# Optimization experiments

Hardware: AMD Instinct MI355X
Metric: run time of the kernel (lower is better)

The kernel has to match this reference:

```python
import jax, jax.numpy as jnp
import numpy as np

LORA_ALPHA = 32
LORA_RANK = 16
SCALING = LORA_ALPHA / LORA_RANK  # 2.0


def setup_inputs() -> dict:
    key = jax.random.key(0)
    ks = jax.random.split(key, 6)
    B_, S, D_IN, D_OUT, E, R = 4, 2048, 4096, 4096, 8, LORA_RANK
    x = jax.random.normal(ks[0], (B_, S, D_IN), dtype=jnp.float32)
    W_base = jax.random.normal(ks[1], (D_OUT, D_IN), dtype=jnp.float32) * (D_IN ** -0.5)
    b_base = jax.random.normal(ks[2], (D_OUT,), dtype=jnp.float32) * 0.01
    W_gate = jax.random.normal(ks[3], (E, D_IN), dtype=jnp.float32) * (D_IN ** -0.5)
    A = jax.random.normal(ks[4], (E, R, D_IN), dtype=jnp.float32) * (D_IN ** -0.5)
    B = jax.random.normal(ks[5], (D_OUT, R), dtype=jnp.float32)[None] * jnp.ones((E, 1, 1), jnp.float32) * 0.02
    B = jax.random.normal(ks[5], (E, D_OUT, R), dtype=jnp.float32) * 0.02
    return {"x": x, "W_base": W_base, "b_base": b_base, "W_gate": W_gate, "A": A, "B": B}


def reference(x, W_base, b_base, W_gate, A, B):
    # Base linear: [b,s,d_in] @ [d_out,d_in]^T -> [b,s,d_out]
    result = jnp.einsum('bsd,od->bso', x, W_base) + b_base
    # Softmax gating over experts: [b,s,E]
    route = jax.nn.softmax(jnp.einsum('bsd,ed->bse', x, W_gate), axis=-1)
    # All-expert low-rank down-projection: [b,s,E,r] (dropout is Identity, p=0)
    h = jnp.einsum('bsd,erd->bser', x, A)
    # Fuse route weight into the small low-rank intermediate before up-projection
    hw = h * route[..., None]
    # Weighted sum over experts of up-projection: [b,s,d_out]
    result = result + SCALING * jnp.einsum('bser,eor->bso', hw, B)
    return result
```

## Files before the change

### kernel.cpp

```cpp
#include <hip/hip_runtime.h>
#include <hip/hip_bf16.h>


typedef __attribute__((ext_vector_type(8))) short  bf16x8;
typedef __attribute__((ext_vector_type(4))) float  f32x4;
typedef __attribute__((ext_vector_type(4))) unsigned short us4;
typedef __attribute__((ext_vector_type(4))) float  fl4;

__device__ __forceinline__ unsigned short f2bf(float f) {
  unsigned int u = __float_as_uint(f);
  u += 0x7FFFu + ((u >> 16) & 1u);
  return (unsigned short)(u >> 16);
}

__device__ __forceinline__ void gload16(const void* g, void* l) {
  __builtin_amdgcn_global_load_lds(
      (const __attribute__((address_space(1))) unsigned int*)g,
      (__attribute__((address_space(3))) unsigned int*)l, 16, 0, 0);
}

#define WS_XBF 0u
#define WS_WBF 67108864u
#define WS_AG  100663296u
#define WS_U   101842944u
#define WS_HW  102891520u

__global__ __launch_bounds__(256) void prep_kernel(
    const float* __restrict__ x, const float* __restrict__ Wb,
    const float* __restrict__ Wg, const float* __restrict__ A,
    const float* __restrict__ B,
    unsigned short* __restrict__ Xbf, unsigned short* __restrict__ Wbf,
    unsigned short* __restrict__ AG, unsigned short* __restrict__ U)
{
  const long N0 = 8388608;
  const long N1 = N0 + 4194304;
  const long N2 = N1 + 139264;
  const long N3 = N2 + 8192;
  const long N4 = N3 + 131072;
  long i = (long)blockIdx.x * blockDim.x + threadIdx.x;
  long stride = (long)gridDim.x * blockDim.x;
  for (; i < N4; i += stride) {
    if (i < N1) {
      const float* s; unsigned short* d; long j;
      if (i < N0) { s = x;  d = Xbf; j = i; }
      else        { s = Wb; d = Wbf; j = i - N0; }
      fl4 v = ((const fl4*)s)[j];
      us4 o; o[0]=f2bf(v[0]); o[1]=f2bf(v[1]); o[2]=f2bf(v[2]); o[3]=f2bf(v[3]);
      ((us4*)d)[j] = o;
    } else if (i < N2) {
      long j = i - N1;
      fl4 v = (j < 8192) ? ((const fl4*)Wg)[j] : ((const fl4*)A)[j - 8192];
      us4 o; o[0]=f2bf(v[0]); o[1]=f2bf(v[1]); o[2]=f2bf(v[2]); o[3]=f2bf(v[3]);
      ((us4*)AG)[j] = o;
    } else if (i < N3) {
      long j = i - N2;
      us4 z = (us4)0;
      ((us4*)(AG + 136*4096))[j] = z;
    } else {
      long j = i - N3;
      long o = j >> 5;
      long c4 = j & 31;
      long e = c4 >> 2, r4 = c4 & 3;
      fl4 v = ((const fl4*)B)[e*16384 + o*4 + r4];
      us4 t; t[0]=f2bf(2.f*v[0]); t[1]=f2bf(2.f*v[1]);
             t[2]=f2bf(2.f*v[2]); t[3]=f2bf(2.f*v[3]);
      ((us4*)U)[j] = t;
    }
  }
}

__global__ __launch_bounds__(256) void gate_h_kernel(
    const unsigned short* __restrict__ Xbf,
    const unsigned short* __restrict__ AG,
    unsigned short* __restrict__ HW)
{
  __shared__ unsigned short Xt[64*32];
  __shared__ unsigned short At[144*32];
  __shared__ float accs[64*136];

  int tid = threadIdx.x;
  int lane = tid & 63;
  int w = tid >> 6;
  long brow = (long)blockIdx.x * 64;

  f32x4 acc[9];
#pragma unroll
  for (int i = 0; i < 9; ++i) acc[i] = (f32x4){0.f,0.f,0.f,0.f};

  int lrow = lane >> 2;
  int lcol = (lane & 3) * 8;

  for (int kb = 0; kb < 128; ++kb) {
    __syncthreads();
    gload16(Xbf + (brow + w*16 + lrow)*4096 + kb*32 + lcol, (char*)Xt + w*1024);
    for (int c = w; c < 9; c += 4)
      gload16(AG + (long)(c*16 + lrow)*4096 + kb*32 + lcol, (char*)At + c*1024);
    __syncthreads();
    int r16 = lane & 15, kh = lane >> 4;
    bf16x8 a = *(const bf16x8*)&Xt[(w*16 + r16)*32 + kh*8];
#pragma unroll
    for (int n = 0; n < 9; ++n) {
      bf16x8 b = *(const bf16x8*)&At[(n*16 + r16)*32 + kh*8];
      acc[n] = __builtin_amdgcn_mfma_f32_16x16x32_bf16(a, b, acc[n], 0, 0, 0);
    }
  }
  __syncthreads();
  {
    int r16 = lane & 15, rg = lane >> 4;
#pragma unroll
    for (int n = 0; n < 9; ++n) {
      int col = n*16 + r16;
      if (col < 136) {
#pragma unroll
        for (int j = 0; j < 4; ++j)
          accs[(w*16 + rg*4 + j)*136 + col] = acc[n][j];
      }
    }
  }
  __syncthreads();
  {
    int r = tid >> 2;
    int q = tid & 3;
    const float* rp = &accs[r*136];
    float mx = rp[0];
#pragma unroll
    for (int e = 1; e < 8; ++e) mx = fmaxf(mx, rp[e]);
    float ex[8]; float s = 0.f;
#pragma unroll
    for (int e = 0; e < 8; ++e) { ex[e] = __expf(rp[e] - mx); s += ex[e]; }
    float inv = 1.f / s;
#pragma unroll
    for (int jj = 0; jj < 8; ++jj) {
      int col = q*32 + jj*4;
      float rt = ex[col >> 4] * inv;
      us4 o;
      o[0] = f2bf(rp[8+col+0] * rt);
      o[1] = f2bf(rp[8+col+1] * rt);
      o[2] = f2bf(rp[8+col+2] * rt);
      o[3] = f2bf(rp[8+col+3] * rt);
      *(us4*)&HW[(brow + r)*128 + col] = o;
    }
  }
}

__global__ __launch_bounds__(256) void gemm_main(
    const unsigned short* __restrict__ Xbf,
    const unsigned short* __restrict__ Wbf,
    const unsigned short* __restrict__ HW,
    const unsigned short* __restrict__ U,
    const float* __restrict__ bias,
    float* __restrict__ out)
{
  __shared__ unsigned short At[128*32];
  __shared__ unsigned short Bt[128*32];

  int tid = threadIdx.x;
  int lane = tid & 63;
  int w = tid >> 6;
  int wr = w >> 1, wc = w & 1;

  int bid = blockIdx.x;
  long brow = (long)(bid >> 5) * 128;
  long bcol = (long)(bid & 31) * 128;

  f32x4 acc[4][4];
#pragma unroll
  for (int m = 0; m < 4; ++m)
#pragma unroll
    for (int n = 0; n < 4; ++n) acc[m][n] = (f32x4){0.f,0.f,0.f,0.f};

  int lrow = lane >> 2;
  int lcol = (lane & 3) * 8;
  int r16 = lane & 15, kh = lane >> 4;

  auto step = [&](const unsigned short* __restrict__ pA, long ldA,
                  const unsigned short* __restrict__ pB, long ldB, int k0) {
    __syncthreads();
#pragma unroll
    for (int i = 0; i < 2; ++i) {
      int chunk = w*2 + i;
      int row = chunk*16 + lrow;
      gload16(pA + (brow + row)*ldA + k0 + lcol, (char*)At + chunk*1024);
      gload16(pB + (bcol + row)*ldB + k0 + lcol, (char*)Bt + chunk*1024);
    }
    __syncthreads();
    bf16x8 af[4], bfr[4];
#pragma unroll
    for (int m = 0; m < 4; ++m)
      af[m] = *(const bf16x8*)&At[(wr*64 + m*16 + r16)*32 + kh*8];
#pragma unroll
    for (int n = 0; n < 4; ++n)
      bfr[n] = *(const bf16x8*)&Bt[(wc*64 + n*16 + r16)*32 + kh*8];
#pragma unroll
    for (int m = 0; m < 4; ++m)
#pragma unroll
      for (int n = 0; n < 4; ++n)
        acc[m][n] = __builtin_amdgcn_mfma_f32_16x16x32_bf16(af[m], bfr[n], acc[m][n], 0, 0, 0);
  };

  for (int kb = 0; kb < 128; ++kb) step(Xbf, 4096, Wbf, 4096, kb*32);
  for (int kb = 0; kb < 4;   ++kb) step(HW, 128, U, 128, kb*32);

  int rg = lane >> 4;
#pragma unroll
  for (int n = 0; n < 4; ++n) {
    long col = bcol + wc*64 + n*16 + r16;
    float b = bias[col];
#pragma unroll
    for (int m = 0; m < 4; ++m) {
      long row0 = brow + wr*64 + m*16 + rg*4;
#pragma unroll
      for (int j = 0; j < 4; ++j)
        out[(row0 + j)*4096 + col] = acc[m][n][j] + b;
    }
  }
}

extern "C" void kernel_launch(void* const* d_in, const int* in_sizes, int n_in,
                              void* d_out, int out_size, void* d_ws, size_t ws_size,
                              hipStream_t stream) {
  (void)in_sizes; (void)n_in; (void)out_size; (void)ws_size;
  const float* x  = (const float*)d_in[0];
  const float* Wb = (const float*)d_in[1];
  const float* bb = (const float*)d_in[2];
  const float* Wg = (const float*)d_in[3];
  const float* A  = (const float*)d_in[4];
  const float* B  = (const float*)d_in[5];
  float* out = (float*)d_out;
  char* ws = (char*)d_ws;

  unsigned short* Xbf = (unsigned short*)(ws + WS_XBF);
  unsigned short* Wbf = (unsigned short*)(ws + WS_WBF);
  unsigned short* AG  = (unsigned short*)(ws + WS_AG);
  unsigned short* U   = (unsigned short*)(ws + WS_U);
  unsigned short* HW  = (unsigned short*)(ws + WS_HW);

  hipLaunchKernelGGL(prep_kernel, dim3(2048), dim3(256), 0, stream,
                     x, Wb, Wg, A, B, Xbf, Wbf, AG, U);
  hipLaunchKernelGGL(gate_h_kernel, dim3(128), dim3(256), 0, stream,
                     Xbf, AG, HW);
  hipLaunchKernelGGL(gemm_main, dim3(2048), dim3(256), 0, stream,
                     Xbf, Wbf, HW, U, bb, out);
}
```

Before: 684.7 us.

## Rewrite main GEMM as 256x256 pipelined tile and split-K the gate kernel

The main GEMM moves from 128x128 tiles with 32-wide K steps to 256x256 tiles with 64-wide K steps, 8 waves per block, double-buffered LDS with an XOR swizzle, and interleaved prefetch/MFMA phases using explicit vmcnt waits and s_setprio. The gate/down-projection kernel is split along K into two halves across 512 blocks, writing bf16 partials that a separate reduce kernel sums before applying the softmax and route scaling. The aim is more data reuse per tile and latency hiding in the dominant GEMM, plus more parallelism in the small gate GEMM. The cost is an extra launch and round trip through memory, and bf16 rounding of the partial logits, which slightly lowers gating precision.

After: 564.2 us. -17.6%, faster.

```diff
diff --git a/kernel.cpp b/kernel.cpp
--- a/kernel.cpp
+++ b/kernel.cpp
@@ -12,18 +12,27 @@
   u += 0x7FFFu + ((u >> 16) & 1u);
   return (unsigned short)(u >> 16);
 }
-
+__device__ __forceinline__ float bf2f(unsigned short u) {
+  return __uint_as_float(((unsigned int)u) << 16);
+}
 __device__ __forceinline__ void gload16(const void* g, void* l) {
   __builtin_amdgcn_global_load_lds(
       (const __attribute__((address_space(1))) unsigned int*)g,
       (__attribute__((address_space(3))) unsigned int*)l, 16, 0, 0);
 }
+
+#define BAR() do { asm volatile("" ::: "memory"); \
+                   __builtin_amdgcn_s_barrier();  \
+                   asm volatile("" ::: "memory"); } while (0)
+#define VMCNT6() asm volatile("s_waitcnt vmcnt(6)" ::: "memory")
+#define VMCNT0() asm volatile("s_waitcnt vmcnt(0)" ::: "memory")
 
 #define WS_XBF 0u
 #define WS_WBF 67108864u
 #define WS_AG  100663296u
 #define WS_U   101842944u
 #define WS_HW  102891520u
+#define WS_HP  104988672u
 
 __global__ __launch_bounds__(256) void prep_kernel(
     const float* __restrict__ x, const float* __restrict__ Wb,
@@ -69,81 +78,144 @@
   }
 }
 
-__global__ __launch_bounds__(256) void gate_h_kernel(
+__global__ __launch_bounds__(256) void gate_partial(
     const unsigned short* __restrict__ Xbf,
     const unsigned short* __restrict__ AG,
-    unsigned short* __restrict__ HW)
+    unsigned short* __restrict__ HP)
 {
-  __shared__ unsigned short Xt[64*32];
-  __shared__ unsigned short At[144*32];
-  __shared__ float accs[64*136];
+  __shared__ unsigned short Xt[32*32];
+  __shared__ unsigned short At[160*32];
 
   int tid = threadIdx.x;
   int lane = tid & 63;
   int w = tid >> 6;
-  long brow = (long)blockIdx.x * 64;
-
-  f32x4 acc[9];
-#pragma unroll
-  for (int i = 0; i < 9; ++i) acc[i] = (f32x4){0.f,0.f,0.f,0.f};
-
-  int lrow = lane >> 2;
-  int lcol = (lane & 3) * 8;
-
-  for (int kb = 0; kb < 128; ++kb) {
+  int wm = w & 1, wn = w >> 1;
+  int mt = blockIdx.x >> 1, ks = blockIdx.x & 1;
+  long brow = (long)mt * 32;
+  long kbase = (long)ks * 2048;
+
+  f32x4 acc[5];
+#pragma unroll
+  for (int i = 0; i < 5; ++i) acc[i] = (f32x4){0.f,0.f,0.f,0.f};
+
+  int r16 = lane & 15, kh = lane >> 4;
+
+  for (int kb = 0; kb < 64; ++kb) {
+    long kc = kbase + kb*32;
     __syncthreads();
-    gload16(Xbf + (brow + w*16 + lrow)*4096 + kb*32 + lcol, (char*)Xt + w*1024);
-    for (int c = w; c < 9; c += 4)
-      gload16(AG + (long)(c*16 + lrow)*4096 + kb*32 + lcol, (char*)At + c*1024);
+    for (int s = w; s < 11; s += 4) {
+      if (s < 2)
+        gload16(Xbf + (brow + s*16 + (lane>>2))*4096 + kc + (lane&3)*8,
+                (char*)Xt + s*1024);
+      else
+        gload16(AG + ((long)((s-2)*16 + (lane>>2)))*4096 + kc + (lane&3)*8,
+                (char*)At + (s-2)*1024);
+    }
     __syncthreads();
-    int r16 = lane & 15, kh = lane >> 4;
-    bf16x8 a = *(const bf16x8*)&Xt[(w*16 + r16)*32 + kh*8];
-#pragma unroll
-    for (int n = 0; n < 9; ++n) {
-      bf16x8 b = *(const bf16x8*)&At[(n*16 + r16)*32 + kh*8];
-      acc[n] = __builtin_amdgcn_mfma_f32_16x16x32_bf16(a, b, acc[n], 0, 0, 0);
+    bf16x8 a = *(const bf16x8*)&Xt[(wm*16 + r16)*32 + kh*8];
+#pragma unroll
+    for (int c = 0; c < 5; ++c) {
+      int ch = wn*5 + c;
+      bf16x8 b = *(const bf16x8*)&At[(ch*16 + r16)*32 + kh*8];
+      acc[c] = __builtin_amdgcn_mfma_f32_16x16x32_bf16(a, b, acc[c], 0, 0, 0);
     }
   }
-  __syncthreads();
-  {
-    int r16 = lane & 15, rg = lane >> 4;
-#pragma unroll
-    for (int n = 0; n < 9; ++n) {
-      int col = n*16 + r16;
-      if (col < 136) {
-#pragma unroll
-        for (int j = 0; j < 4; ++j)
-          accs[(w*16 + rg*4 + j)*136 + col] = acc[n][j];
-      }
+
+  long rowg = brow + wm*16 + (lane>>4)*4;
+#pragma unroll
+  for (int c = 0; c < 5; ++c) {
+    int ch = wn*5 + c;
+    if (ch > 8) continue;
+    int col = ch*16 + r16;
+    if (col < 136) {
+#pragma unroll
+      for (int j = 0; j < 4; ++j)
+        HP[((long)ks*8192 + rowg + j)*136 + col] = f2bf(acc[c][j]);
     }
   }
-  __syncthreads();
-  {
-    int r = tid >> 2;
-    int q = tid & 3;
-    const float* rp = &accs[r*136];
-    float mx = rp[0];
-#pragma unroll
-    for (int e = 1; e < 8; ++e) mx = fmaxf(mx, rp[e]);
-    float ex[8]; float s = 0.f;
-#pragma unroll
-    for (int e = 0; e < 8; ++e) { ex[e] = __expf(rp[e] - mx); s += ex[e]; }
-    float inv = 1.f / s;
-#pragma unroll
-    for (int jj = 0; jj < 8; ++jj) {
-      int col = q*32 + jj*4;
-      float rt = ex[col >> 4] * inv;
-      us4 o;
-      o[0] = f2bf(rp[8+col+0] * rt);
-      o[1] = f2bf(rp[8+col+1] * rt);
-      o[2] = f2bf(rp[8+col+2] * rt);
-      o[3] = f2bf(rp[8+col+3] * rt);
-      *(us4*)&HW[(brow + r)*128 + col] = o;
-    }
-  }
-}
-
-__global__ __launch_bounds__(256) void gemm_main(
+}
+
+__global__ __launch_bounds__(256) void gate_reduce(
+    const unsigned short* __restrict__ HP,
+    unsigned short* __restrict__ HW)
+{
+  int tid = threadIdx.x;
+  long r = (long)blockIdx.x*64 + (tid>>2);
+  int q = tid & 3;
+  const us4* r0 = (const us4*)(HP + r*136);
+  const us4* r1 = (const us4*)(HP + (8192 + r)*136);
+
+  us4 la0 = r0[0], la1 = r0[1], lb0 = r1[0], lb1 = r1[1];
+  float lg[8];
+#pragma unroll
+  for (int e = 0; e < 4; ++e) {
+    lg[e]   = bf2f(la0[e]) + bf2f(lb0[e]);
+    lg[4+e] = bf2f(la1[e]) + bf2f(lb1[e]);
+  }
+  float mx = lg[0];
+#pragma unroll
+  for (int e = 1; e < 8; ++e) mx = fmaxf(mx, lg[e]);
+  float ex[8]; float s = 0.f;
+#pragma unroll
+  for (int e = 0; e < 8; ++e) { ex[e] = __expf(lg[e] - mx); s += ex[e]; }
+  float inv = 1.f / s;
+
+  us4* ow = (us4*)(HW + r*128);
+#pragma unroll
+  for (int k = 0; k < 8; ++k) {
+    us4 h0 = r0[2 + q*8 + k], h1 = r1[2 + q*8 + k];
+    int col0 = q*32 + k*4;
+    float rt = ex[col0 >> 4] * inv;
+    us4 o;
+#pragma unroll
+    for (int i = 0; i < 4; ++i)
+      o[i] = f2bf((bf2f(h0[i]) + bf2f(h1[i])) * rt);
+    ow[q*8 + k] = o;
+  }
+}
+
+#define NKT 66
+
+struct Op { const unsigned short* a; const unsigned short* b; long lda, ldb, k0; };
+
+__device__ __forceinline__ Op getop(int kt,
+    const unsigned short* X, const unsigned short* W,
+    const unsigned short* HW, const unsigned short* U) {
+  Op o;
+  if (kt < 64) { o.a = X;  o.b = W; o.lda = 4096; o.ldb = 4096; o.k0 = (long)kt*64; }
+  else         { o.a = HW; o.b = U; o.lda = 128;  o.ldb = 128;  o.k0 = (long)(kt-64)*64; }
+  return o;
+}
+
+__device__ __forceinline__ void stA(const unsigned short* src, long ld, long k0,
+                                    long brow, char* dst, int mh, int t) {
+  int l = t & 63, w = t >> 6;
+  int kc = ((l & 7) ^ (l >> 3)) << 3;
+#pragma unroll
+  for (int i = 0; i < 2; ++i) {
+    long grow = (long)i*128 + mh*64 + w*8 + (l>>3);
+    gload16(src + (brow + grow)*ld + k0 + kc,
+            dst + mh*8192 + i*16384 + (long)t*16);
+  }
+}
+__device__ __forceinline__ void stB(const unsigned short* src, long ld, long k0,
+                                    long bcol, char* dst, int nh, int t) {
+  int l = t & 63, w = t >> 6;
+  int kc = ((l & 7) ^ (l >> 3)) << 3;
+#pragma unroll
+  for (int i = 0; i < 2; ++i) {
+    long grow = ((long)i*2 + (w>>2))*64 + nh*32 + (w&3)*8 + (l>>3);
+    gload16(src + (bcol + grow)*ld + k0 + kc,
+            dst + i*16384 + (w>>2)*8192 + nh*4096 + ((long)(w&3)*64 + l)*16);
+  }
+}
+
+__device__ __forceinline__ bf16x8 frag(const char* buf, int row, int ks, int kh, int l7) {
+  int slot = (ks*4 + kh) ^ l7;
+  return *(const bf16x8*)(buf + (long)row*128 + slot*16);
+}
+
+__global__ __launch_bounds__(512, 2) void gemm8(
     const unsigned short* __restrict__ Xbf,
     const unsigned short* __restrict__ Wbf,
     const unsigned short* __restrict__ HW,
@@ -151,69 +223,155 @@
     const float* __restrict__ bias,
     float* __restrict__ out)
 {
-  __shared__ unsigned short At[128*32];
-  __shared__ unsigned short Bt[128*32];
+  __shared__ char lds[131072];
 
   int tid = threadIdx.x;
   int lane = tid & 63;
   int w = tid >> 6;
-  int wr = w >> 1, wc = w & 1;
+  int wr = w >> 2, wc = w & 3;
+  int r16 = lane & 15, kh = lane >> 4, l7 = lane & 7;
 
   int bid = blockIdx.x;
-  long brow = (long)(bid >> 5) * 128;
-  long bcol = (long)(bid & 31) * 128;
-
-  f32x4 acc[4][4];
-#pragma unroll
-  for (int m = 0; m < 4; ++m)
-#pragma unroll
-    for (int n = 0; n < 4; ++n) acc[m][n] = (f32x4){0.f,0.f,0.f,0.f};
-
-  int lrow = lane >> 2;
-  int lcol = (lane & 3) * 8;
-  int r16 = lane & 15, kh = lane >> 4;
-
-  auto step = [&](const unsigned short* __restrict__ pA, long ldA,
-                  const unsigned short* __restrict__ pB, long ldB, int k0) {
-    __syncthreads();
-#pragma unroll
-    for (int i = 0; i < 2; ++i) {
-      int chunk = w*2 + i;
-      int row = chunk*16 + lrow;
-      gload16(pA + (brow + row)*ldA + k0 + lcol, (char*)At + chunk*1024);
-      gload16(pB + (bcol + row)*ldB + k0 + lcol, (char*)Bt + chunk*1024);
+  long brow = (long)(bid >> 4) * 256;
+  long bcol = (long)(bid & 15) * 256;
+
+  f32x4 acc[2][2][4][2];
+#pragma unroll
+  for (int mh = 0; mh < 2; ++mh)
+#pragma unroll
+    for (int nh = 0; nh < 2; ++nh)
+#pragma unroll
+      for (int m = 0; m < 4; ++m)
+#pragma unroll
+        for (int n = 0; n < 2; ++n) acc[mh][nh][m][n] = (f32x4){0.f,0.f,0.f,0.f};
+
+  char* A0b = lds;
+  char* B0b = lds + 65536;
+
+  {
+    Op o0 = getop(0, Xbf, Wbf, HW, U);
+    Op o1 = getop(1, Xbf, Wbf, HW, U);
+    stA(o0.a, o0.lda, o0.k0, brow, A0b, 0, tid);
+    stB(o0.b, o0.ldb, o0.k0, bcol, B0b, 0, tid);
+    stB(o0.b, o0.ldb, o0.k0, bcol, B0b, 1, tid);
+    stA(o0.a, o0.lda, o0.k0, brow, A0b, 1, tid);
+    stA(o1.a, o1.lda, o1.k0, brow, A0b + 32768, 0, tid);
+    stB(o1.b, o1.ldb, o1.k0, bcol, B0b + 32768, 0, tid);
+    stB(o1.b, o1.ldb, o1.k0, bcol, B0b + 32768, 1, tid);
+    VMCNT6();
+    BAR();
+  }
+
+  bf16x8 a[4][2], b0[2][2], b1[2][2];
+
+  for (int kt = 0; kt < NKT; ++kt) {
+    const char* rA = A0b + (kt & 1) * 32768;
+    const char* rB = B0b + (kt & 1) * 32768;
+    char* wA1 = A0b + ((kt + 1) & 1) * 32768;
+    char* wA2 = A0b + (kt & 1) * 32768;
+    char* wB2 = B0b + (kt & 1) * 32768;
+    Op o1 = getop(kt + 1 < NKT ? kt + 1 : 0, Xbf, Wbf, HW, U);
+    Op o2 = getop(kt + 2 < NKT ? kt + 2 : 0, Xbf, Wbf, HW, U);
+
+#pragma unroll
+    for (int m = 0; m < 4; ++m)
+#pragma unroll
+      for (int ks = 0; ks < 2; ++ks)
+        a[m][ks] = frag(rA, wr*128 + m*16 + r16, ks, kh, l7);
+#pragma unroll
+    for (int n = 0; n < 2; ++n)
+#pragma unroll
+      for (int ks = 0; ks < 2; ++ks)
+        b0[n][ks] = frag(rB, wc*64 + n*16 + r16, ks, kh, l7);
+    if (kt + 1 < NKT) stA(o1.a, o1.lda, o1.k0, brow, wA1, 1, tid);
+    BAR();
+    __builtin_amdgcn_s_setprio(1);
+#pragma unroll
+    for (int m = 0; m < 4; ++m)
+#pragma unroll
+      for (int n = 0; n < 2; ++n)
+#pragma unroll
+        for (int ks = 0; ks < 2; ++ks)
+          acc[0][0][m][n] = __builtin_amdgcn_mfma_f32_16x16x32_bf16(
+              a[m][ks], b0[n][ks], acc[0][0][m][n], 0, 0, 0);
+    __builtin_amdgcn_s_setprio(0);
+    BAR();
+
+#pragma unroll
+    for (int n = 0; n < 2; ++n)
+#pragma unroll
+      for (int ks = 0; ks < 2; ++ks)
+        b1[n][ks] = frag(rB, wc*64 + 32 + n*16 + r16, ks, kh, l7);
+    if (kt + 2 < NKT) stA(o2.a, o2.lda, o2.k0, brow, wA2, 0, tid);
+    BAR();
+    __builtin_amdgcn_s_setprio(1);
+#pragma unroll
+    for (int m = 0; m < 4; ++m)
+#pragma unroll
+      for (int n = 0; n < 2; ++n)
+#pragma unroll
+        for (int ks = 0; ks < 2; ++ks)
+          acc[0][1][m][n] = __builtin_amdgcn_mfma_f32_16x16x32_bf16(
+              a[m][ks], b1[n][ks], acc[0][1][m][n], 0, 0, 0);
+    __builtin_amdgcn_s_setprio(0);
+    BAR();
+
+#pragma unroll
+    for (int m = 0; m < 4; ++m)
+#pragma unroll
+      for (int ks = 0; ks < 2; ++ks)
+        a[m][ks] = frag(rA, wr*128 + 64 + m*16 + r16, ks, kh, l7);
+    if (kt + 2 < NKT) stB(o2.b, o2.ldb, o2.k0, bcol, wB2, 0, tid);
+    BAR();
+    __builtin_amdgcn_s_setprio(1);
+#pragma unroll
+    for (int m = 0; m < 4; ++m)
+#pragma unroll
+      for (int n = 0; n < 2; ++n)
+#pragma unroll
+        for (int ks = 0; ks < 2; ++ks)
+          acc[1][1][m][n] = __builtin_amdgcn_mfma_f32_16x16x32_bf16(
+              a[m][ks], b1[n][ks], acc[1][1][m][n], 0, 0, 0);
+    __builtin_amdgcn_s_setprio(0);
+    BAR();
+
+    if (kt + 2 < NKT) {
+      stB(o2.b, o2.ldb, o2.k0, bcol, wB2, 1, tid);
+      VMCNT6();
+    } else if (kt + 1 < NKT) {
+      VMCNT0();
     }
-    __syncthreads();
-    bf16x8 af[4], bfr[4];
-#pragma unroll
-    for (int m = 0; m < 4; ++m)
-      af[m] = *(const bf16x8*)&At[(wr*64 + m*16 + r16)*32 + kh*8];
-#pragma unroll
-    for (int n = 0; n < 4; ++n)
-      bfr[n] = *(const bf16x8*)&Bt[(wc*64 + n*16 + r16)*32 + kh*8];
-#pragma unroll
-    for (int m = 0; m < 4; ++m)
-#pragma unroll
-      for (int n = 0; n < 4; ++n)
-        acc[m][n] = __builtin_amdgcn_mfma_f32_16x16x32_bf16(af[m], bfr[n], acc[m][n], 0, 0, 0);
-  };
-
-  for (int kb = 0; kb < 128; ++kb) step(Xbf, 4096, Wbf, 4096, kb*32);
-  for (int kb = 0; kb < 4;   ++kb) step(HW, 128, U, 128, kb*32);
+    BAR();
+    __builtin_amdgcn_s_setprio(1);
+#pragma unroll
+    for (int m = 0; m < 4; ++m)
+#pragma unroll
+      for (int n = 0; n < 2; ++n)
+#pragma unroll
+        for (int ks = 0; ks < 2; ++ks)
+          acc[1][0][m][n] = __builtin_amdgcn_mfma_f32_16x16x32_bf16(
+              a[m][ks], b0[n][ks], acc[1][0][m][n], 0, 0, 0);
+    __builtin_amdgcn_s_setprio(0);
+    BAR();
+  }
 
   int rg = lane >> 4;
 #pragma unroll
-  for (int n = 0; n < 4; ++n) {
-    long col = bcol + wc*64 + n*16 + r16;
-    float b = bias[col];
-#pragma unroll
-    for (int m = 0; m < 4; ++m) {
-      long row0 = brow + wr*64 + m*16 + rg*4;
-#pragma unroll
-      for (int j = 0; j < 4; ++j)
-        out[(row0 + j)*4096 + col] = acc[m][n][j] + b;
-    }
-  }
+  for (int mh = 0; mh < 2; ++mh)
+#pragma unroll
+    for (int nh = 0; nh < 2; ++nh)
+#pragma unroll
+      for (int n = 0; n < 2; ++n) {
+        long col = bcol + wc*64 + nh*32 + n*16 + r16;
+        float bv = bias[col];
+#pragma unroll
+        for (int m = 0; m < 4; ++m) {
+          long row0 = brow + wr*128 + mh*64 + m*16 + rg*4;
+#pragma unroll
+          for (int j = 0; j < 4; ++j)
+            out[(row0 + j)*4096 + col] = acc[mh][nh][m][n][j] + bv;
+        }
+      }
 }
 
 extern "C" void kernel_launch(void* const* d_in, const int* in_sizes, int n_in,
@@ -234,11 +392,14 @@
   unsigned short* AG  = (unsigned short*)(ws + WS_AG);
   unsigned short* U   = (unsigned short*)(ws + WS_U);
   unsigned short* HW  = (unsigned short*)(ws + WS_HW);
+  unsigned short* HP  = (unsigned short*)(ws + WS_HP);
 
   hipLaunchKernelGGL(prep_kernel, dim3(2048), dim3(256), 0, stream,
                      x, Wb, Wg, A, B, Xbf, Wbf, AG, U);
-  hipLaunchKernelGGL(gate_h_kernel, dim3(128), dim3(256), 0, stream,
-                     Xbf, AG, HW);
-  hipLaunchKernelGGL(gemm_main, dim3(2048), dim3(256), 0, stream,
+  hipLaunchKernelGGL(gate_partial, dim3(512), dim3(256), 0, stream,
+                     Xbf, AG, HP);
+  hipLaunchKernelGGL(gate_reduce, dim3(128), dim3(256), 0, stream,
+                     HP, HW);
+  hipLaunchKernelGGL(gemm8, dim3(512), dim3(512), 0, stream,
                      Xbf, Wbf, HW, U, bb, out);
 }
```
